# Optimization experiments

Hardware: AMD Instinct MI355X
Metric: run time of the kernel (lower is better)

Reference implementation:

```python
import jax, jax.numpy as jnp
import numpy as np

SERIES_LEN = 4096
D_EMB = 1024
D_V = 1024
HURST = 0.7
H = HURST - 0.5          # exponent used by the module
DT = 1.0 / SERIES_LEN
EPS = 1e-8


def _attn_matrix():
    # Lower-triangular fractional power-law matrix A2[i, j]:
    #   j <  i : ((i - j) * dt + 1e-8) ** (hurst - 0.5)
    #   j == i : 1e-8 ** (hurst - 0.5)
    #   j >  i : 0
    i = jnp.arange(SERIES_LEN, dtype=jnp.int32)[:, None]
    j = jnp.arange(SERIES_LEN, dtype=jnp.int32)[None, :]
    diff = jnp.clip(i - j, 1, None).astype(jnp.float32)  # safe base for fractional power
    lower = jnp.where(i > j, (diff * DT + EPS) ** H, 0.0)
    diag = jnp.eye(SERIES_LEN, dtype=jnp.float32) * (EPS ** H)
    return lower + diag  # (L, L) float32


def setup_inputs() -> dict:
    key = jax.random.key(0)
    k1, k2 = jax.random.split(key)
    embed_series = jax.random.normal(k1, (D_EMB, SERIES_LEN), dtype=jnp.float32)
    # nn.Linear(d_emb, d_v, bias=False) weight has shape (d_v, d_emb)
    Wv_weight = jax.random.normal(k2, (D_V, D_EMB), dtype=jnp.float32) * (1.0 / np.sqrt(D_EMB))
    return {"embed_series": embed_series, "Wv_weight": Wv_weight}


def reference(embed_series, Wv_weight):
    # V (original, d_v x L) = Wv(embed_series.T).T ; output[i, c] = sum_j A2[i, j] * V[c, j]
    # => out = A2 @ (embed_series.T @ Wv_weight.T), shape (L, d_v)
    A2 = _attn_matrix()                                   # (L, L) lower triangular
    Y = jnp.einsum('el,ve->lv', embed_series, Wv_weight)  # (L, d_v)
    return A2 @ Y                                         # (L, d_v)
```

## Files before the change

kernel.cpp:

```cpp
#include <hip/hip_runtime.h>
#include <hip/hip_bf16.h>
#include <cstdint>
#include <cstddef>


#define L_SER 4096
#define DEMB  1024
#define DV    1024

#define R_STRIDE 4224
#define R_O0     4096

typedef __bf16 bf16_t;
typedef __attribute__((ext_vector_type(8))) __bf16 bf16x8;
typedef __attribute__((ext_vector_type(4))) float f32x4;

__device__ __forceinline__ void glds16(const bf16_t* g, bf16_t* l) {
    __builtin_amdgcn_global_load_lds(
        (const __attribute__((address_space(1))) unsigned int*)(const void*)g,
        (__attribute__((address_space(3))) unsigned int*)(void*)l,
        16, 0, 0);
}

__global__ void prep_kernel(const float* __restrict__ E, const float* __restrict__ W,
                            bf16_t* __restrict__ Eb, bf16_t* __restrict__ Wb,
                            bf16_t* __restrict__ R) {
    const int b = blockIdx.x;
    if (b < 132) {
        int idx = b * 256 + threadIdx.x;
        int s = idx / R_STRIDE;
        int x = idx - s * R_STRIDE;
        int d = R_O0 + s - x;
        float v = 0.0f;
        if (d >= 0 && d < L_SER)
            v = powf((d == 0) ? 1e-8f : ((float)d * (1.0f / (float)L_SER) + 1e-8f), 0.2f);
        R[idx] = (bf16_t)v;
    } else if (b < 132 + 2048) {
        int idx = (b - 132) * 256 + threadIdx.x;
        const f32x4* s = (const f32x4*)E;
        f32x4 v0 = s[idx * 2], v1 = s[idx * 2 + 1];
        bf16x8 o;
        o[0] = (bf16_t)v0[0]; o[1] = (bf16_t)v0[1]; o[2] = (bf16_t)v0[2]; o[3] = (bf16_t)v0[3];
        o[4] = (bf16_t)v1[0]; o[5] = (bf16_t)v1[1]; o[6] = (bf16_t)v1[2]; o[7] = (bf16_t)v1[3];
        ((bf16x8*)Eb)[idx] = o;
    } else {
        int idx = (b - 2180) * 256 + threadIdx.x;
        const f32x4* s = (const f32x4*)W;
        f32x4 v0 = s[idx * 2], v1 = s[idx * 2 + 1];
        bf16x8 o;
        o[0] = (bf16_t)v0[0]; o[1] = (bf16_t)v0[1]; o[2] = (bf16_t)v0[2]; o[3] = (bf16_t)v0[3];
        o[4] = (bf16_t)v1[0]; o[5] = (bf16_t)v1[1]; o[6] = (bf16_t)v1[2]; o[7] = (bf16_t)v1[3];
        ((bf16x8*)Wb)[idx] = o;
    }
}

#define GA_STAGE(SBOFS)                                                      \
    _Pragma("unroll")                                                        \
    for (int c = 0; c < 4; ++c) {                                            \
        glds16(pA[c], &sA[(SBOFS) + (c * 32 + wave * 8) * 64]);              \
        glds16(pB[c], &sB[(SBOFS) + (c * 32 + wave * 8) * 64]);              \
        pA[c] += 64; pB[c] += 64;                                            \
    }

#define GA_COMPUTE(SBOFS)                                                    \
    _Pragma("unroll")                                                        \
    for (int kk = 0; kk < 2; ++kk) {                                         \
        const int co = kk ? coff1 : coff0;                                   \
        bf16x8 afr[4], bfr[4];                                               \
        _Pragma("unroll")                                                    \
        for (int tm = 0; tm < 4; ++tm)                                       \
            afr[tm] = *(const bf16x8*)&sA[(SBOFS) + (wm * 64 + tm * 16 + ln) * 64 + co]; \
        _Pragma("unroll")                                                    \
        for (int tn = 0; tn < 4; ++tn)                                       \
            bfr[tn] = *(const bf16x8*)&sB[(SBOFS) + (wn * 64 + tn * 16 + ln) * 64 + co]; \
        _Pragma("unroll")                                                    \
        for (int tm = 0; tm < 4; ++tm)                                       \
            _Pragma("unroll")                                                \
            for (int tn = 0; tn < 4; ++tn)                                   \
                acc[tm][tn] = __builtin_amdgcn_mfma_f32_16x16x32_bf16(afr[tm], bfr[tn], acc[tm][tn], 0, 0, 0); \
    }

#define GA_LANES()                                                           \
    const int tid  = threadIdx.x;                                            \
    const int wave = tid >> 6;                                               \
    const int lane = tid & 63;                                               \
    const int quad = lane >> 4;                                              \
    const int ln   = lane & 15;                                              \
    const int wm   = wave >> 1;                                              \
    const int wn   = wave & 1;                                               \
    const int lrow = lane >> 3;                                              \
    const int lch  = (lane & 7) ^ lrow;                                      \
    const int rsw   = ln & 7;                                                \
    const int coff0 = ((quad ^ rsw)) * 8;                                    \
    const int coff1 = (((4 + quad) ^ rsw)) * 8;

__global__ __launch_bounds__(256, 2) void gemm_a_kernel(const bf16_t* __restrict__ R,
                                                        const bf16_t* __restrict__ Eb,
                                                        bf16_t* __restrict__ T0,
                                                        bf16_t* __restrict__ T1) {
    __shared__ __align__(16) bf16_t sA[2 * 128 * 64];
    __shared__ __align__(16) bf16_t sB[2 * 128 * 64];

    const int bid = blockIdx.x;
    int I, nb, h;
    if (bid < 256) { I = bid >> 3;                nb = bid & 7;         h = 0; }
    else           { I = 31 - ((bid - 256) >> 3); nb = (bid - 256) & 7; h = 1; }
    const int i0 = I * 128;
    const int n0 = nb * 128;
    const int nsteps = I + 1;
    const int j0b = h ? 64 * (I + 1) : 0;
    bf16_t* __restrict__ Tout = h ? T1 : T0;

    GA_LANES()

    f32x4 acc[4][4];
#pragma unroll
    for (int a = 0; a < 4; ++a)
#pragma unroll
        for (int b = 0; b < 4; ++b) acc[a][b] = (f32x4){0, 0, 0, 0};

    const bf16_t* pA[4];
    const bf16_t* pB[4];
#pragma unroll
    for (int c = 0; c < 4; ++c) {
        int r = c * 32 + wave * 8 + lrow;
        pA[c] = R + (size_t)(r & 7) * R_STRIDE + (R_O0 - i0 + j0b - 8 * (r >> 3) + lch * 8);
        pB[c] = Eb + (size_t)(n0 + r) * L_SER + j0b + lch * 8;
    }

    GA_STAGE(0)
    for (int s = 0;; s += 2) {
        __syncthreads();
        if (s + 1 < nsteps) { GA_STAGE(128 * 64) }
        GA_COMPUTE(0)
        if (s + 1 >= nsteps) break;
        __syncthreads();
        if (s + 2 < nsteps) { GA_STAGE(0) }
        GA_COMPUTE(128 * 64)
        if (s + 2 >= nsteps) break;
    }

#pragma unroll
    for (int tm = 0; tm < 4; ++tm) {
        int row_base = i0 + wm * 64 + tm * 16 + quad * 4;
#pragma unroll
        for (int tn = 0; tn < 4; ++tn) {
            int col = n0 + wn * 64 + tn * 16 + ln;
#pragma unroll
            for (int r = 0; r < 4; ++r)
                Tout[(size_t)(row_base + r) * DEMB + col] = (bf16_t)acc[tm][tn][r];
        }
    }
}

#define GB_COMPUTE(SBOFS)                                                    \
    _Pragma("unroll")                                                        \
    for (int kk = 0; kk < 2; ++kk) {                                         \
        const int co = kk ? coff1 : coff0;                                   \
        bf16x8 afr[4], bfr[4];                                               \
        _Pragma("unroll")                                                    \
        for (int c = 0; c < 4; ++c)                                          \
            afr[c] = *(const bf16x8*)&sA[(SBOFS) + (((c >> 1) * 64) + wm * 32 + (c & 1) * 16 + ln) * 64 + co]; \
        _Pragma("unroll")                                                    \
        for (int tn = 0; tn < 4; ++tn)                                       \
            bfr[tn] = *(const bf16x8*)&sB[(SBOFS) + (wn * 64 + tn * 16 + ln) * 64 + co]; \
        _Pragma("unroll")                                                    \
        for (int t = 0; t < 2; ++t)                                          \
            _Pragma("unroll")                                                \
            for (int tn = 0; tn < 4; ++tn)                                   \
                acc[t][tn] = __builtin_amdgcn_mfma_f32_16x16x32_bf16(afr[t], bfr[tn], acc[t][tn], 0, 0, 0); \
        _Pragma("unroll")                                                    \
        for (int t = 0; t < 2; ++t)                                          \
            _Pragma("unroll")                                                \
            for (int tn = 0; tn < 4; ++tn)                                   \
                acc[t][tn] = __builtin_amdgcn_mfma_f32_16x16x32_bf16(afr[2 + t], bfr[tn], acc[t][tn], 0, 0, 0); \
    }

__global__ __launch_bounds__(256, 2) void gemm_b_kernel(const bf16_t* __restrict__ T0,
                                                        const bf16_t* __restrict__ T1,
                                                        const bf16_t* __restrict__ Wb,
                                                        float* __restrict__ out) {
    __shared__ __align__(16) bf16_t sA[2 * 128 * 64];
    __shared__ __align__(16) bf16_t sB[2 * 128 * 64];

    const int bid = blockIdx.x;
    const int ib = bid >> 3;
    const int nb = bid & 7;
    const int i0 = ib * 64;
    const int n0 = nb * 128;

    GA_LANES()

    f32x4 acc[2][4];
#pragma unroll
    for (int a = 0; a < 2; ++a)
#pragma unroll
        for (int b = 0; b < 4; ++b) acc[a][b] = (f32x4){0, 0, 0, 0};

    const int nsteps = DEMB / 64;

    const bf16_t* pA[4];
    const bf16_t* pB[4];
#pragma unroll
    for (int c = 0; c < 4; ++c) {
        const bf16_t* base = (c < 2) ? T0 : T1;
        int rr = (c & 1) * 32 + wave * 8 + lrow;
        pA[c] = base + (size_t)(i0 + rr) * DEMB + lch * 8;
        pB[c] = Wb + (size_t)(n0 + c * 32 + wave * 8 + lrow) * DEMB + lch * 8;
    }

    GA_STAGE(0)
    for (int s = 0;; s += 2) {
        __syncthreads();
        if (s + 1 < nsteps) { GA_STAGE(128 * 64) }
        GB_COMPUTE(0)
        if (s + 1 >= nsteps) break;
        __syncthreads();
        if (s + 2 < nsteps) { GA_STAGE(0) }
        GB_COMPUTE(128 * 64)
        if (s + 2 >= nsteps) break;
    }

#pragma unroll
    for (int t = 0; t < 2; ++t) {
        int row_base = i0 + wm * 32 + t * 16 + quad * 4;
#pragma unroll
        for (int tn = 0; tn < 4; ++tn) {
            int col = n0 + wn * 64 + tn * 16 + ln;
#pragma unroll
            for (int r = 0; r < 4; ++r)
                out[(size_t)(row_base + r) * DV + col] = acc[t][tn][r];
        }
    }
}

extern "C" void kernel_launch(void* const* d_in, const int* in_sizes, int n_in,
                              void* d_out, int out_size, void* d_ws, size_t ws_size,
                              hipStream_t stream) {
    const float* E = (const float*)d_in[0];
    const float* W = (const float*)d_in[1];
    float* out = (float*)d_out;

    char* ws = (char*)d_ws;
    bf16_t* Eb = (bf16_t*)(ws);
    bf16_t* T0 = (bf16_t*)(ws + (size_t)8  * 1024 * 1024);
    bf16_t* T1 = (bf16_t*)(ws + (size_t)16 * 1024 * 1024);
    bf16_t* Wb = (bf16_t*)(ws + (size_t)24 * 1024 * 1024);
    bf16_t* R  = (bf16_t*)(ws + (size_t)26 * 1024 * 1024);

    prep_kernel<<<2692, 256, 0, stream>>>(E, W, Eb, Wb, R);
    gemm_a_kernel<<<512, 256, 0, stream>>>(R, Eb, T0, T1);
    gemm_b_kernel<<<512, 256, 0, stream>>>(T0, T1, Wb, out);
}
```

Measured before the change: 125.0 us.

## Load Toeplitz A and W operands directly from global instead of LDS

In gemm_a, the Toeplitz power-law operand is no longer staged through shared memory. Each lane reads its MFMA fragments straight from the small, cache-resident R table. In gemm_b, the weight operand fragments are likewise read directly from global memory per lane rather than staged in LDS. This halves LDS footprint and staging traffic, which may allow higher occupancy, but it exposes global and L2 load latency inside the MFMA loop without software prefetch.

```diff
diff --git a/kernel.cpp b/kernel.cpp
--- a/kernel.cpp
+++ b/kernel.cpp
@@ -54,32 +54,6 @@
     }
 }
 
-#define GA_STAGE(SBOFS)                                                      \
-    _Pragma("unroll")                                                        \
-    for (int c = 0; c < 4; ++c) {                                            \
-        glds16(pA[c], &sA[(SBOFS) + (c * 32 + wave * 8) * 64]);              \
-        glds16(pB[c], &sB[(SBOFS) + (c * 32 + wave * 8) * 64]);              \
-        pA[c] += 64; pB[c] += 64;                                            \
-    }
-
-#define GA_COMPUTE(SBOFS)                                                    \
-    _Pragma("unroll")                                                        \
-    for (int kk = 0; kk < 2; ++kk) {                                         \
-        const int co = kk ? coff1 : coff0;                                   \
-        bf16x8 afr[4], bfr[4];                                               \
-        _Pragma("unroll")                                                    \
-        for (int tm = 0; tm < 4; ++tm)                                       \
-            afr[tm] = *(const bf16x8*)&sA[(SBOFS) + (wm * 64 + tm * 16 + ln) * 64 + co]; \
-        _Pragma("unroll")                                                    \
-        for (int tn = 0; tn < 4; ++tn)                                       \
-            bfr[tn] = *(const bf16x8*)&sB[(SBOFS) + (wn * 64 + tn * 16 + ln) * 64 + co]; \
-        _Pragma("unroll")                                                    \
-        for (int tm = 0; tm < 4; ++tm)                                       \
-            _Pragma("unroll")                                                \
-            for (int tn = 0; tn < 4; ++tn)                                   \
-                acc[tm][tn] = __builtin_amdgcn_mfma_f32_16x16x32_bf16(afr[tm], bfr[tn], acc[tm][tn], 0, 0, 0); \
-    }
-
 #define GA_LANES()                                                           \
     const int tid  = threadIdx.x;                                            \
     const int wave = tid >> 6;                                               \
@@ -94,11 +68,36 @@
     const int coff0 = ((quad ^ rsw)) * 8;                                    \
     const int coff1 = (((4 + quad) ^ rsw)) * 8;
 
+#define GA_STAGE_B(SBOFS)                                                    \
+    _Pragma("unroll")                                                        \
+    for (int c = 0; c < 4; ++c) {                                            \
+        glds16(pB[c], &sB[(SBOFS) + (c * 32 + wave * 8) * 64]);              \
+        pB[c] += 64;                                                         \
+    }
+
+#define GA_COMPUTE(SBOFS)                                                    \
+    _Pragma("unroll")                                                        \
+    for (int kk = 0; kk < 2; ++kk) {                                         \
+        const int co = kk ? coff1 : coff0;                                   \
+        bf16x8 afr[4], bfr[4];                                               \
+        _Pragma("unroll")                                                    \
+        for (int tm = 0; tm < 4; ++tm)                                       \
+            afr[tm] = *(const bf16x8*)(pRA + (kk * 32 + quad * 8 - 16 * tm)); \
+        _Pragma("unroll")                                                    \
+        for (int tn = 0; tn < 4; ++tn)                                       \
+            bfr[tn] = *(const bf16x8*)&sB[(SBOFS) + (wn * 64 + tn * 16 + ln) * 64 + co]; \
+        _Pragma("unroll")                                                    \
+        for (int tm = 0; tm < 4; ++tm)                                       \
+            _Pragma("unroll")                                                \
+            for (int tn = 0; tn < 4; ++tn)                                   \
+                acc[tm][tn] = __builtin_amdgcn_mfma_f32_16x16x32_bf16(afr[tm], bfr[tn], acc[tm][tn], 0, 0, 0); \
+    }                                                                        \
+    pRA += 64;
+
 __global__ __launch_bounds__(256, 2) void gemm_a_kernel(const bf16_t* __restrict__ R,
                                                         const bf16_t* __restrict__ Eb,
                                                         bf16_t* __restrict__ T0,
                                                         bf16_t* __restrict__ T1) {
-    __shared__ __align__(16) bf16_t sA[2 * 128 * 64];
     __shared__ __align__(16) bf16_t sB[2 * 128 * 64];
 
     const int bid = blockIdx.x;
@@ -119,23 +118,23 @@
 #pragma unroll
         for (int b = 0; b < 4; ++b) acc[a][b] = (f32x4){0, 0, 0, 0};
 
-    const bf16_t* pA[4];
+    const bf16_t* pRA = R + (size_t)(ln & 7) * R_STRIDE +
+                        (R_O0 - i0 + j0b - 64 * wm - 8 * (ln >> 3) + 48);
+    pRA -= 48;
+
     const bf16_t* pB[4];
 #pragma unroll
-    for (int c = 0; c < 4; ++c) {
-        int r = c * 32 + wave * 8 + lrow;
-        pA[c] = R + (size_t)(r & 7) * R_STRIDE + (R_O0 - i0 + j0b - 8 * (r >> 3) + lch * 8);
-        pB[c] = Eb + (size_t)(n0 + r) * L_SER + j0b + lch * 8;
-    }
-
-    GA_STAGE(0)
+    for (int c = 0; c < 4; ++c)
+        pB[c] = Eb + (size_t)(n0 + c * 32 + wave * 8 + lrow) * L_SER + j0b + lch * 8;
+
+    GA_STAGE_B(0)
     for (int s = 0;; s += 2) {
         __syncthreads();
-        if (s + 1 < nsteps) { GA_STAGE(128 * 64) }
+        if (s + 1 < nsteps) { GA_STAGE_B(128 * 64) }
         GA_COMPUTE(0)
         if (s + 1 >= nsteps) break;
         __syncthreads();
-        if (s + 2 < nsteps) { GA_STAGE(0) }
+        if (s + 2 < nsteps) { GA_STAGE_B(0) }
         GA_COMPUTE(128 * 64)
         if (s + 2 >= nsteps) break;
     }
@@ -153,6 +152,13 @@
     }
 }
 
+#define GB_STAGE_A(SBOFS)                                                    \
+    _Pragma("unroll")                                                        \
+    for (int c = 0; c < 4; ++c) {                                            \
+        glds16(pA[c], &sA[(SBOFS) + (c * 32 + wave * 8) * 64]);              \
+        pA[c] += 64;                                                         \
+    }
+
 #define GB_COMPUTE(SBOFS)                                                    \
     _Pragma("unroll")                                                        \
     for (int kk = 0; kk < 2; ++kk) {                                         \
@@ -163,7 +169,7 @@
             afr[c] = *(const bf16x8*)&sA[(SBOFS) + (((c >> 1) * 64) + wm * 32 + (c & 1) * 16 + ln) * 64 + co]; \
         _Pragma("unroll")                                                    \
         for (int tn = 0; tn < 4; ++tn)                                       \
-            bfr[tn] = *(const bf16x8*)&sB[(SBOFS) + (wn * 64 + tn * 16 + ln) * 64 + co]; \
+            bfr[tn] = *(const bf16x8*)(pWg[tn] + kk * 32 + quad * 8);        \
         _Pragma("unroll")                                                    \
         for (int t = 0; t < 2; ++t)                                          \
             _Pragma("unroll")                                                \
@@ -174,14 +180,15 @@
             _Pragma("unroll")                                                \
             for (int tn = 0; tn < 4; ++tn)                                   \
                 acc[t][tn] = __builtin_amdgcn_mfma_f32_16x16x32_bf16(afr[2 + t], bfr[tn], acc[t][tn], 0, 0, 0); \
-    }
+    }                                                                        \
+    _Pragma("unroll")                                                        \
+    for (int tn = 0; tn < 4; ++tn) pWg[tn] += 64;
 
 __global__ __launch_bounds__(256, 2) void gemm_b_kernel(const bf16_t* __restrict__ T0,
                                                         const bf16_t* __restrict__ T1,
                                                         const bf16_t* __restrict__ Wb,
                                                         float* __restrict__ out) {
     __shared__ __align__(16) bf16_t sA[2 * 128 * 64];
-    __shared__ __align__(16) bf16_t sB[2 * 128 * 64];
 
     const int bid = blockIdx.x;
     const int ib = bid >> 3;
@@ -200,23 +207,25 @@
     const int nsteps = DEMB / 64;
 
     const bf16_t* pA[4];
-    const bf16_t* pB[4];
 #pragma unroll
     for (int c = 0; c < 4; ++c) {
         const bf16_t* base = (c < 2) ? T0 : T1;
         int rr = (c & 1) * 32 + wave * 8 + lrow;
         pA[c] = base + (size_t)(i0 + rr) * DEMB + lch * 8;
-        pB[c] = Wb + (size_t)(n0 + c * 32 + wave * 8 + lrow) * DEMB + lch * 8;
-    }
-
-    GA_STAGE(0)
+    }
+    const bf16_t* pWg[4];
+#pragma unroll
+    for (int tn = 0; tn < 4; ++tn)
+        pWg[tn] = Wb + (size_t)(n0 + wn * 64 + tn * 16 + ln) * DEMB;
+
+    GB_STAGE_A(0)
     for (int s = 0;; s += 2) {
         __syncthreads();
-        if (s + 1 < nsteps) { GA_STAGE(128 * 64) }
+        if (s + 1 < nsteps) { GB_STAGE_A(128 * 64) }
         GB_COMPUTE(0)
         if (s + 1 >= nsteps) break;
         __syncthreads();
-        if (s + 2 < nsteps) { GA_STAGE(0) }
+        if (s + 2 < nsteps) { GB_STAGE_A(0) }
         GB_COMPUTE(128 * 64)
         if (s + 2 >= nsteps) break;
     }
```

After: 146.8 us. 17.4% more time.
